# Kernel optimization log

Hardware: AMD Instinct MI355X
Metric: run time of the kernel (lower is better)

The kernel has to match this reference:

```python
import jax, jax.numpy as jnp
import numpy as np

N_FFT = 1024
HOP = 256
WIN = 1024
N_MELS = 80
SR = 22050
F_MIN = 0.0
CUTOFF = N_FFT // 2 + 1  # 513
PAD = (N_FFT - HOP) // 2  # 384
LOG_CLIP = 1e-5
B, T = 32, 262144


def _hann_periodic(n):
    return (0.5 - 0.5 * np.cos(2.0 * np.pi * np.arange(n) / n)).astype(np.float64)


def _hz_to_mel(f):
    f = np.atleast_1d(np.asarray(f, dtype=np.float64))
    f_sp = 200.0 / 3
    mels = f / f_sp
    min_log_hz = 1000.0
    min_log_mel = min_log_hz / f_sp
    logstep = np.log(6.4) / 27.0
    log_t = f >= min_log_hz
    mels[log_t] = min_log_mel + np.log(f[log_t] / min_log_hz) / logstep
    return mels


def _mel_to_hz(m):
    m = np.asarray(m, dtype=np.float64)
    f_sp = 200.0 / 3
    freqs = m * f_sp
    min_log_hz = 1000.0
    min_log_mel = min_log_hz / f_sp
    logstep = np.log(6.4) / 27.0
    log_t = m >= min_log_mel
    freqs = np.where(log_t, min_log_hz * np.exp(logstep * (m - min_log_mel)), freqs)
    return freqs


def _mel_filterbank(sr, n_fft, n_mels, fmin, fmax):
    # librosa.filters.mel with htk=False, norm='slaney'
    if fmax is None:
        fmax = sr / 2.0
    mel_f = _mel_to_hz(np.linspace(_hz_to_mel(fmin)[0], _hz_to_mel(fmax)[0], n_mels + 2))
    fftfreqs = np.linspace(0.0, sr / 2.0, 1 + n_fft // 2)
    fdiff = np.diff(mel_f)
    ramps = mel_f[:, None] - fftfreqs[None, :]
    lower = -ramps[:-2] / fdiff[:-1, None]
    upper = ramps[2:] / fdiff[1:, None]
    weights = np.maximum(0.0, np.minimum(lower, upper))
    enorm = 2.0 / (mel_f[2:n_mels + 2] - mel_f[:n_mels])
    weights *= enorm[:, None]
    return weights.astype(np.float32)  # [n_mels, cutoff]


def _forward_basis():
    # Windowed real/imag DFT basis, as in the torch module.
    fourier = np.fft.fft(np.eye(N_FFT))
    basis = np.vstack([np.real(fourier[:CUTOFF, :]), np.imag(fourier[:CUTOFF, :])])
    basis = basis * _hann_periodic(WIN)[None, :]
    return basis.astype(np.float32)  # [2*cutoff, n_fft]


def setup_inputs() -> dict:
    key = jax.random.key(0)
    audio = jax.random.uniform(key, (B, T), dtype=jnp.float32, minval=-1.0, maxval=1.0)
    return {
        "audio": audio,
        "forward_basis": jnp.asarray(_forward_basis()),
        "mel_basis": jnp.asarray(_mel_filterbank(SR, N_FFT, N_MELS, F_MIN, None)),
        "jitter_steps": 0,
    }


def reference(audio, forward_basis, mel_basis, jitter_steps):
    # jitter_steps == 0 at eval: no random shift applied.
    padded = jnp.pad(audio, ((0, 0), (PAD, PAD)), mode="reflect")  # [B, T+2*PAD]
    n_frames = (padded.shape[-1] - N_FFT) // HOP + 1
    idx = jnp.arange(n_frames)[:, None] * HOP + jnp.arange(N_FFT)[None, :]
    frames = padded[:, idx]  # [B, n_frames, n_fft]
    ft = jnp.einsum("btn,cn->bct", frames, forward_basis)  # [B, 2*cutoff, n_frames]
    real, imag = ft[:, :CUTOFF, :], ft[:, CUTOFF:, :]
    mag = jnp.sqrt(real * real + imag * imag)  # [B, cutoff, n_frames]
    mel = jnp.einsum("mc,bct->bmt", mel_basis, mag)  # [B, n_mels, n_frames]
    return jnp.log(jnp.clip(mel, LOG_CLIP, None))
```

## Files before the change

kernel.cpp:

```cpp
#include <hip/hip_runtime.h>
#include <hip/hip_bf16.h>

typedef short bf16x8 __attribute__((ext_vector_type(8)));
typedef float f32x4  __attribute__((ext_vector_type(4)));
typedef int   i32x4  __attribute__((ext_vector_type(4)));

#define T_AUDIO 262144
#define PADL 384
#define CUTOFF 513
#define CPAD 576
#define NMELS 80
#define SEGLEN 33536
#define EBYTES 33536

__device__ __forceinline__ unsigned short f2bf(float f){
  union { float f; unsigned u; } v; v.f = f;
  return (unsigned short)((v.u + 0x7FFFu + ((v.u >> 16) & 1u)) >> 16);
}

__device__ __forceinline__ void gload_lds16(const void* g, void* l){
  __builtin_amdgcn_global_load_lds(
      (const __attribute__((address_space(1))) unsigned int*)g,
      (__attribute__((address_space(3))) unsigned int*)l, 16, 0, 0);
}

__global__ void k_extra(const float* __restrict__ audio,
                        const float* __restrict__ basis,
                        unsigned short* __restrict__ magT){
  __shared__ float swr[4], swi[4];
  int tid = threadIdx.x;
  int gid = blockIdx.x * 256 + tid;
  int b   = gid >> 17;
  int rem = gid & 131071;
  int t   = rem >> 7;
  int k0  = (rem & 127) << 3;
  int s0  = t * 256 + k0 - PADL;
  const float* ap = audio + (long)b * T_AUDIO;
  float v[8];
  if (s0 >= 0 && s0 + 7 < T_AUDIO){
    f32x4 a0 = *(const f32x4*)(ap + s0);
    f32x4 a1 = *(const f32x4*)(ap + s0 + 4);
    v[0]=a0[0]; v[1]=a0[1]; v[2]=a0[2]; v[3]=a0[3];
    v[4]=a1[0]; v[5]=a1[1]; v[6]=a1[2]; v[7]=a1[3];
  } else {
    #pragma unroll
    for (int e = 0; e < 8; ++e){
      int s = s0 + e;
      if (s < 0) s = -s;
      if (s >= T_AUDIO) s = 2*(T_AUDIO-1) - s;
      v[e] = ap[s];
    }
  }
  const float* r256 = basis + 256 * 1024 + k0;
  const float* i256 = basis + 769 * 1024 + k0;
  float dr = 0.f, di = 0.f;
  #pragma unroll
  for (int e = 0; e < 8; ++e){ dr += v[e]*r256[e]; di += v[e]*i256[e]; }
  #pragma unroll
  for (int off = 32; off; off >>= 1){
    dr += __shfl_down(dr, off, 64);
    di += __shfl_down(di, off, 64);
  }
  int lane = tid & 63, wid = tid >> 6;
  if (lane == 0){ swr[wid] = dr; swi[wid] = di; }
  __syncthreads();
  long tg = (long)b * 1024 + t;
  if (tid == 0 || tid == 128){
    float R = (tid == 0) ? (swr[0] + swr[1]) : (swr[2] + swr[3]);
    float I = (tid == 0) ? (swi[0] + swi[1]) : (swi[2] + swi[3]);
    magT[tg * CPAD + 256] = f2bf(sqrtf(R*R + I*I));
  }
  int c = tid & 127;
  if (c < 63){
    int p = (c < 7) ? (257 + c) : (513 + c);
    magT[tg * CPAD + p] = 0;
  }
}

__global__ void k_basis4(const float* __restrict__ basis, unsigned short* __restrict__ bi2f){
  int CI = blockIdx.x * 256 + threadIdx.x;
  int l  = CI & 63;
  int f  = (CI >> 6) & 7;
  int s  = (CI >> 9) & 15;
  int p  = (CI >> 13) & 1;
  int g  = CI >> 14;
  int R  = g * 128 + (f >> 2) * 64 + (f & 3) * 16 + (l & 15);
  int srcr = (R >> 1) + 513 * (R & 1);
  const float* sp = basis + srcr * 1024 + 2 * (s * 32 + (l >> 4) * 8) + p;
  bf16x8 o;
  #pragma unroll
  for (int e = 0; e < 8; ++e) o[e] = (short)f2bf(sp[2*e]);
  *(bf16x8*)(bi2f + (long)CI * 8) = o;
}

__global__ void k_w(const float* __restrict__ w, unsigned short* __restrict__ wb){
  int gid = blockIdx.x * 256 + threadIdx.x;
  if (gid >= NMELS * CPAD) return;
  int m = gid / CPAD, p = gid % CPAD;
  float v = 0.f;
  if (p <= 256) v = w[m * CUTOFF + p];
  else if (p >= 264 && p <= 519) v = w[m * CUTOFF + (p - 7)];
  wb[gid] = f2bf(v);
}

__launch_bounds__(256, 2)
__global__ void k_stft(const unsigned short* __restrict__ bi2f,
                       const float* __restrict__ audio,
                       unsigned short* __restrict__ magT){
  __shared__ __align__(16) char LDS[2 * EBYTES];
  const int tid = threadIdx.x;
  const int l   = tid & 63, w = tid >> 6;
  const int wm  = w >> 1, wn = w & 1;
  const int x   = l & 15, h = l >> 4;

  int bx = blockIdx.x;
  int sw = ((bx & 7) << 7) | (bx >> 3);
  const int g  = sw & 3;
  const int nt = sw >> 2;

  {
    const long segbase = (long)(nt >> 3) * T_AUDIO;
    const int  f0 = (nt & 7) << 7;
    const int  sstart = f0 * 256 - PADL;
    const float* ap = audio + segbase;
    #pragma unroll
    for (int it = 0; it < 17; ++it){
      int p0 = (it * 256 + tid) * 8;
      if (p0 < SEGLEN){
        int sg = sstart + p0;
        float v[8];
        if (sg >= 0 && sg + 7 < T_AUDIO){
          f32x4 a0 = *(const f32x4*)(ap + sg);
          f32x4 a1 = *(const f32x4*)(ap + sg + 4);
          v[0]=a0[0]; v[1]=a0[1]; v[2]=a0[2]; v[3]=a0[3];
          v[4]=a1[0]; v[5]=a1[1]; v[6]=a1[2]; v[7]=a1[3];
        } else {
          #pragma unroll
          for (int e = 0; e < 8; ++e){
            int ss = sg + e;
            if (ss < 0) ss = -ss;
            if (ss >= T_AUDIO) ss = 2*(T_AUDIO-1) - ss;
            v[e] = ap[ss];
          }
        }
        unsigned long long pe = (unsigned long long)f2bf(v[0])
                              | ((unsigned long long)f2bf(v[2]) << 16)
                              | ((unsigned long long)f2bf(v[4]) << 32)
                              | ((unsigned long long)f2bf(v[6]) << 48);
        unsigned long long po = (unsigned long long)f2bf(v[1])
                              | ((unsigned long long)f2bf(v[3]) << 16)
                              | ((unsigned long long)f2bf(v[5]) << 32)
                              | ((unsigned long long)f2bf(v[7]) << 48);
        int ep = p0 >> 1;
        int C  = ep >> 3;
        int ad = ((C ^ ((C >> 4) & 15)) << 4) + ((ep & 4) << 1);
        *(unsigned long long*)(LDS + ad)          = pe;
        *(unsigned long long*)(LDS + EBYTES + ad) = po;
      }
    }
  }
  __syncthreads();

  const char* AgE = (const char*)bi2f + (long)(g * 256 + wm * 4) * 1024 + l * 16;
  const char* AgO = AgE + 131072;

  int C0[4];
  #pragma unroll
  for (int j = 0; j < 4; ++j) C0[j] = (wn * 64 + j * 16 + x) * 16 + h;

  f32x4 accE[4][4] = {}, accO[4][4] = {};
  bf16x8 aE[2][4], aO[2][4];
  #pragma unroll
  for (int i = 0; i < 4; ++i){
    aE[0][i] = *(const bf16x8*)(AgE + i * 1024);
    aO[0][i] = *(const bf16x8*)(AgO + i * 1024);
  }

  #pragma unroll
  for (int s = 0; s < 16; ++s){
    const int cur = s & 1, nxt = cur ^ 1;
    if (s < 15){
      #pragma unroll
      for (int i = 0; i < 4; ++i){
        aE[nxt][i] = *(const bf16x8*)(AgE + (s + 1) * 8192 + i * 1024);
        aO[nxt][i] = *(const bf16x8*)(AgO + (s + 1) * 8192 + i * 1024);
      }
    }
    bf16x8 bqE[4], bqO[4];
    #pragma unroll
    for (int j = 0; j < 4; ++j){
      int C  = C0[j] + s * 4;
      int ad = (C ^ ((C >> 4) & 15)) << 4;
      bqE[j] = *(const bf16x8*)(LDS + ad);
      bqO[j] = *(const bf16x8*)(LDS + EBYTES + ad);
    }
    __builtin_amdgcn_s_setprio(1);
    #pragma unroll
    for (int i = 0; i < 4; ++i)
      #pragma unroll
      for (int j = 0; j < 4; ++j)
        accE[i][j] = __builtin_amdgcn_mfma_f32_16x16x32_bf16(aE[cur][i], bqE[j], accE[i][j], 0, 0, 0);
    #pragma unroll
    for (int i = 0; i < 4; ++i)
      #pragma unroll
      for (int j = 0; j < 4; ++j)
        accO[i][j] = __builtin_amdgcn_mfma_f32_16x16x32_bf16(aO[cur][i], bqO[j], accO[i][j], 0, 0, 0);
    __builtin_amdgcn_s_setprio(0);
  }

  __syncthreads();
  #pragma unroll
  for (int i = 0; i < 4; ++i){
    int cp1 = wm * 16 + i * 4 + h;
    int mp  = 63 - cp1;
    #pragma unroll
    for (int j = 0; j < 4; ++j){
      int tl = wn * 64 + j * 16 + x;
      f32x4 E = accE[i][j], O = accO[i][j];
      float m1 = sqrtf((E[0]+O[0])*(E[0]+O[0]) + (E[1]+O[1])*(E[1]+O[1]));
      float m2 = sqrtf((E[2]+O[2])*(E[2]+O[2]) + (E[3]+O[3])*(E[3]+O[3]));
      float m3 = sqrtf((E[0]-O[0])*(E[0]-O[0]) + (E[1]-O[1])*(E[1]-O[1]));
      float m4 = sqrtf((E[2]-O[2])*(E[2]-O[2]) + (E[3]-O[3])*(E[3]-O[3]));
      unsigned p1 = (unsigned)f2bf(m1) | ((unsigned)f2bf(m2) << 16);
      unsigned p2 = (unsigned)f2bf(m4) | ((unsigned)f2bf(m3) << 16);
      int xs = (tl & 7) << 2;
      *(unsigned*)(LDS + tl * 256 + ((cp1 ^ xs) << 2)) = p1;
      *(unsigned*)(LDS + tl * 256 + ((mp  ^ xs) << 2)) = p2;
    }
  }
  __syncthreads();

  {
    const long rowbase = (long)(nt * 128) * CPAD;
    int slot8 = tid & 15, rr = tid >> 4;
    int cb0 = (slot8 < 8) ? (64 * g + slot8 * 8) : (392 - 64 * g + slot8 * 8);
    #pragma unroll
    for (int pass = 0; pass < 8; ++pass){
      int tl = pass * 16 + rr;
      int f4 = (slot8 * 4) ^ ((tl & 7) << 2);
      i32x4 vv = *(const i32x4*)(LDS + tl * 256 + f4 * 4);
      *(i32x4*)((char*)magT + (rowbase + (long)tl * CPAD + cb0) * 2) = vv;
    }
  }
}

__launch_bounds__(256)
__global__ void k_mel(const unsigned short* __restrict__ wb,
                      const unsigned short* __restrict__ magT,
                      float* __restrict__ out){
  __shared__ unsigned short Ws[80 * 32];
  __shared__ unsigned short Ms[128 * 32];
  int tid  = threadIdx.x, lane = tid & 63, wid = tid >> 6;
  int bx   = blockIdx.x;
  int bt   = bx & 7, b = bx >> 3;
  int t0   = bt * 128;
  f32x4 acc[5][2] = {};
  const char* Mb = (const char*)(magT + ((long)b * 1024 + t0) * CPAD);
  const char* Wb = (const char*)wb;

  for (int kt = 0; kt < 18; ++kt){
    int k0b = kt * 64;
    {
      int o = tid * 16;
      gload_lds16(Wb + (o >> 6) * 1152 + k0b + (o & 63), (char*)Ws + wid * 1024);
      if (wid == 0){
        int o2 = 4096 + lane * 16;
        gload_lds16(Wb + (o2 >> 6) * 1152 + k0b + (o2 & 63), (char*)Ws + 4096);
      }
    }
    #pragma unroll
    for (int q = 0; q < 2; ++q){
      int o = (q * 256 + tid) * 16;
      gload_lds16(Mb + (long)(o >> 6) * 1152 + k0b + (o & 63), (char*)Ms + q * 4096 + wid * 1024);
    }
    __syncthreads();
    bf16x8 af[5], bfr[2];
    int kb = (lane >> 4) << 4;
    #pragma unroll
    for (int i = 0; i < 5; ++i)
      af[i] = *(const bf16x8*)((const char*)Ws + (i*16 + (lane & 15)) * 64 + kb);
    #pragma unroll
    for (int j = 0; j < 2; ++j)
      bfr[j] = *(const bf16x8*)((const char*)Ms + (wid*32 + j*16 + (lane & 15)) * 64 + kb);
    #pragma unroll
    for (int i = 0; i < 5; ++i)
      #pragma unroll
      for (int j = 0; j < 2; ++j)
        acc[i][j] = __builtin_amdgcn_mfma_f32_16x16x32_bf16(af[i], bfr[j], acc[i][j], 0, 0, 0);
    __syncthreads();
  }
  #pragma unroll
  for (int i = 0; i < 5; ++i)
    #pragma unroll
    for (int j = 0; j < 2; ++j){
      int m = i*16 + ((lane >> 4) << 2);
      int t = t0 + wid*32 + j*16 + (lane & 15);
      #pragma unroll
      for (int r = 0; r < 4; ++r){
        float v = acc[i][j][r];
        out[((long)b * NMELS + (m + r)) * 1024 + t] = logf(fmaxf(v, 1e-5f));
      }
    }
}

__global__ void k_sentinel(float* out, int n){
  int i = blockIdx.x * 256 + threadIdx.x;
  if (i < n) out[i] = 12345.0f;
}

extern "C" void kernel_launch(void* const* d_in, const int* in_sizes, int n_in,
                              void* d_out, int out_size, void* d_ws, size_t ws_size,
                              hipStream_t stream){
  const float* audio = (const float*)d_in[0];
  const float* basis = (const float*)d_in[1];
  const float* melw  = (const float*)d_in[2];
  float* out = (float*)d_out;

  size_t off_bi  = 0;
  size_t off_wb  = (size_t)1024 * 1024;
  size_t off_mag = off_wb + (size_t)NMELS * CPAD * 2;
  size_t total   = off_mag + (size_t)32 * 1024 * CPAD * 2;

  if (ws_size < total){
    k_sentinel<<<(out_size + 255) / 256, 256, 0, stream>>>(out, out_size);
    return;
  }
  char* ws = (char*)d_ws;
  unsigned short* bi2f = (unsigned short*)(ws + off_bi);
  unsigned short* wb   = (unsigned short*)(ws + off_wb);
  unsigned short* magT = (unsigned short*)(ws + off_mag);

  k_extra <<<16384, 256, 0, stream>>>(audio, basis, magT);
  k_basis4<<<  256, 256, 0, stream>>>(basis, bi2f);
  k_w     <<<  180, 256, 0, stream>>>(melw, wb);
  k_stft  <<< 1024, 256, 0, stream>>>(bi2f, audio, magT);
  k_mel   <<<  256, 256, 0, stream>>>(wb, magT, out);
}
```

Before: 81.13 us.

## Double STFT frame tile per block to 256 frames, halving block count

```diff
diff --git a/kernel.cpp b/kernel.cpp
--- a/kernel.cpp
+++ b/kernel.cpp
@@ -10,8 +10,8 @@
 #define CUTOFF 513
 #define CPAD 576
 #define NMELS 80
-#define SEGLEN 33536
-#define EBYTES 33536
+#define SEGLEN2 66304
+#define EB2 66304
 
 __device__ __forceinline__ unsigned short f2bf(float f){
   union { float f; unsigned u; } v; v.f = f;
@@ -103,30 +103,29 @@
   wb[gid] = f2bf(v);
 }
 
-__launch_bounds__(256, 2)
+__launch_bounds__(256, 1)
 __global__ void k_stft(const unsigned short* __restrict__ bi2f,
                        const float* __restrict__ audio,
                        unsigned short* __restrict__ magT){
-  __shared__ __align__(16) char LDS[2 * EBYTES];
+  __shared__ __align__(16) char LDS[2 * EB2];
   const int tid = threadIdx.x;
   const int l   = tid & 63, w = tid >> 6;
   const int wm  = w >> 1, wn = w & 1;
   const int x   = l & 15, h = l >> 4;
 
   int bx = blockIdx.x;
-  int sw = ((bx & 7) << 7) | (bx >> 3);
-  const int g  = sw & 3;
-  const int nt = sw >> 2;
+  int sw = ((bx & 7) << 6) | (bx >> 3);
+  const int g   = sw & 3;
+  const int nt2 = sw >> 2;
 
   {
-    const long segbase = (long)(nt >> 3) * T_AUDIO;
-    const int  f0 = (nt & 7) << 7;
-    const int  sstart = f0 * 256 - PADL;
+    const long segbase = (long)(nt2 >> 2) * T_AUDIO;
+    const int  sstart  = ((nt2 & 3) << 16) - PADL;
     const float* ap = audio + segbase;
-    #pragma unroll
-    for (int it = 0; it < 17; ++it){
+    #pragma unroll 4
+    for (int it = 0; it < 33; ++it){
       int p0 = (it * 256 + tid) * 8;
-      if (p0 < SEGLEN){
+      if (p0 < SEGLEN2){
         int sg = sstart + p0;
         float v[8];
         if (sg >= 0 && sg + 7 < T_AUDIO){
@@ -154,8 +153,8 @@
         int ep = p0 >> 1;
         int C  = ep >> 3;
         int ad = ((C ^ ((C >> 4) & 15)) << 4) + ((ep & 4) << 1);
-        *(unsigned long long*)(LDS + ad)          = pe;
-        *(unsigned long long*)(LDS + EBYTES + ad) = po;
+        *(unsigned long long*)(LDS + ad)       = pe;
+        *(unsigned long long*)(LDS + EB2 + ad) = po;
       }
     }
   }
@@ -164,11 +163,11 @@
   const char* AgE = (const char*)bi2f + (long)(g * 256 + wm * 4) * 1024 + l * 16;
   const char* AgO = AgE + 131072;
 
-  int C0[4];
-  #pragma unroll
-  for (int j = 0; j < 4; ++j) C0[j] = (wn * 64 + j * 16 + x) * 16 + h;
-
-  f32x4 accE[4][4] = {}, accO[4][4] = {};
+  int C0[8];
+  #pragma unroll
+  for (int j = 0; j < 8; ++j) C0[j] = (wn * 128 + j * 16 + x) * 16 + h;
+
+  f32x4 accE[4][8] = {}, accO[4][8] = {};
   bf16x8 aE[2][4], aO[2][4];
   #pragma unroll
   for (int i = 0; i < 4; ++i){
@@ -186,24 +185,32 @@
         aO[nxt][i] = *(const bf16x8*)(AgO + (s + 1) * 8192 + i * 1024);
       }
     }
-    bf16x8 bqE[4], bqO[4];
-    #pragma unroll
-    for (int j = 0; j < 4; ++j){
+    bf16x8 bqE[8];
+    #pragma unroll
+    for (int j = 0; j < 8; ++j){
       int C  = C0[j] + s * 4;
       int ad = (C ^ ((C >> 4) & 15)) << 4;
       bqE[j] = *(const bf16x8*)(LDS + ad);
-      bqO[j] = *(const bf16x8*)(LDS + EBYTES + ad);
     }
     __builtin_amdgcn_s_setprio(1);
     #pragma unroll
     for (int i = 0; i < 4; ++i)
       #pragma unroll
-      for (int j = 0; j < 4; ++j)
+      for (int j = 0; j < 8; ++j)
         accE[i][j] = __builtin_amdgcn_mfma_f32_16x16x32_bf16(aE[cur][i], bqE[j], accE[i][j], 0, 0, 0);
+    __builtin_amdgcn_s_setprio(0);
+    bf16x8 bqO[8];
+    #pragma unroll
+    for (int j = 0; j < 8; ++j){
+      int C  = C0[j] + s * 4;
+      int ad = (C ^ ((C >> 4) & 15)) << 4;
+      bqO[j] = *(const bf16x8*)(LDS + EB2 + ad);
+    }
+    __builtin_amdgcn_s_setprio(1);
     #pragma unroll
     for (int i = 0; i < 4; ++i)
       #pragma unroll
-      for (int j = 0; j < 4; ++j)
+      for (int j = 0; j < 8; ++j)
         accO[i][j] = __builtin_amdgcn_mfma_f32_16x16x32_bf16(aO[cur][i], bqO[j], accO[i][j], 0, 0, 0);
     __builtin_amdgcn_s_setprio(0);
   }
@@ -214,8 +221,8 @@
     int cp1 = wm * 16 + i * 4 + h;
     int mp  = 63 - cp1;
     #pragma unroll
-    for (int j = 0; j < 4; ++j){
-      int tl = wn * 64 + j * 16 + x;
+    for (int j = 0; j < 8; ++j){
+      int tl = wn * 128 + j * 16 + x;
       f32x4 E = accE[i][j], O = accO[i][j];
       float m1 = sqrtf((E[0]+O[0])*(E[0]+O[0]) + (E[1]+O[1])*(E[1]+O[1]));
       float m2 = sqrtf((E[2]+O[2])*(E[2]+O[2]) + (E[3]+O[3])*(E[3]+O[3]));
@@ -231,11 +238,11 @@
   __syncthreads();
 
   {
-    const long rowbase = (long)(nt * 128) * CPAD;
+    const long rowbase = (long)(nt2 * 256) * CPAD;
     int slot8 = tid & 15, rr = tid >> 4;
     int cb0 = (slot8 < 8) ? (64 * g + slot8 * 8) : (392 - 64 * g + slot8 * 8);
     #pragma unroll
-    for (int pass = 0; pass < 8; ++pass){
+    for (int pass = 0; pass < 16; ++pass){
       int tl = pass * 16 + rr;
       int f4 = (slot8 * 4) ^ ((tl & 7) << 2);
       i32x4 vv = *(const i32x4*)(LDS + tl * 256 + f4 * 4);
@@ -333,6 +340,6 @@
   k_extra <<<16384, 256, 0, stream>>>(audio, basis, magT);
   k_basis4<<<  256, 256, 0, stream>>>(basis, bi2f);
   k_w     <<<  180, 256, 0, stream>>>(melw, wb);
-  k_stft  <<< 1024, 256, 0, stream>>>(bi2f, audio, magT);
+  k_stft  <<<  512, 256, 0, stream>>>(bi2f, audio, magT);
   k_mel   <<<  256, 256, 0, stream>>>(wb, magT, out);
 }
```

After: 107.6 us. 1.33x slower.

## Pre-convert audio to bf16 even/odd planes and async-load them into LDS

Applied to the files above, without the earlier changes.

```diff
diff --git a/kernel.cpp b/kernel.cpp
--- a/kernel.cpp
+++ b/kernel.cpp
@@ -12,10 +12,15 @@
 #define NMELS 80
 #define SEGLEN 33536
 #define EBYTES 33536
+#define PCH 16448
+#define PBYTES (PCH*16)
 
 __device__ __forceinline__ unsigned short f2bf(float f){
   union { float f; unsigned u; } v; v.f = f;
   return (unsigned short)((v.u + 0x7FFFu + ((v.u >> 16) & 1u)) >> 16);
+}
+__device__ __forceinline__ float bf2f(unsigned short u){
+  union { unsigned u; float f; } v; v.u = (unsigned)u << 16; return v.f;
 }
 
 __device__ __forceinline__ void gload_lds16(const void* g, void* l){
@@ -24,57 +29,38 @@
       (__attribute__((address_space(3))) unsigned int*)l, 16, 0, 0);
 }
 
-__global__ void k_extra(const float* __restrict__ audio,
-                        const float* __restrict__ basis,
-                        unsigned short* __restrict__ magT){
-  __shared__ float swr[4], swi[4];
-  int tid = threadIdx.x;
-  int gid = blockIdx.x * 256 + tid;
-  int b   = gid >> 17;
-  int rem = gid & 131071;
-  int t   = rem >> 7;
-  int k0  = (rem & 127) << 3;
-  int s0  = t * 256 + k0 - PADL;
+__global__ void k_audio(const float* __restrict__ audio, unsigned short* __restrict__ planes){
+  int bx = blockIdx.x;
+  int b  = bx / 65;
+  int ci = (bx % 65) * 256 + threadIdx.x;
+  if (ci >= PCH) return;
   const float* ap = audio + (long)b * T_AUDIO;
-  float v[8];
-  if (s0 >= 0 && s0 + 7 < T_AUDIO){
-    f32x4 a0 = *(const f32x4*)(ap + s0);
-    f32x4 a1 = *(const f32x4*)(ap + s0 + 4);
-    v[0]=a0[0]; v[1]=a0[1]; v[2]=a0[2]; v[3]=a0[3];
-    v[4]=a1[0]; v[5]=a1[1]; v[6]=a1[2]; v[7]=a1[3];
+  int s0 = 16 * ci - 384;
+  float v[16];
+  if (s0 >= 0 && s0 + 15 < T_AUDIO){
+    #pragma unroll
+    for (int q = 0; q < 4; ++q){
+      f32x4 a = *(const f32x4*)(ap + s0 + q * 4);
+      v[q*4]=a[0]; v[q*4+1]=a[1]; v[q*4+2]=a[2]; v[q*4+3]=a[3];
+    }
   } else {
     #pragma unroll
-    for (int e = 0; e < 8; ++e){
+    for (int e = 0; e < 16; ++e){
       int s = s0 + e;
       if (s < 0) s = -s;
       if (s >= T_AUDIO) s = 2*(T_AUDIO-1) - s;
       v[e] = ap[s];
     }
   }
-  const float* r256 = basis + 256 * 1024 + k0;
-  const float* i256 = basis + 769 * 1024 + k0;
-  float dr = 0.f, di = 0.f;
-  #pragma unroll
-  for (int e = 0; e < 8; ++e){ dr += v[e]*r256[e]; di += v[e]*i256[e]; }
-  #pragma unroll
-  for (int off = 32; off; off >>= 1){
-    dr += __shfl_down(dr, off, 64);
-    di += __shfl_down(di, off, 64);
-  }
-  int lane = tid & 63, wid = tid >> 6;
-  if (lane == 0){ swr[wid] = dr; swi[wid] = di; }
-  __syncthreads();
-  long tg = (long)b * 1024 + t;
-  if (tid == 0 || tid == 128){
-    float R = (tid == 0) ? (swr[0] + swr[1]) : (swr[2] + swr[3]);
-    float I = (tid == 0) ? (swi[0] + swi[1]) : (swi[2] + swi[3]);
-    magT[tg * CPAD + 256] = f2bf(sqrtf(R*R + I*I));
-  }
-  int c = tid & 127;
-  if (c < 63){
-    int p = (c < 7) ? (257 + c) : (513 + c);
-    magT[tg * CPAD + p] = 0;
-  }
+  bf16x8 ev, ov;
+  #pragma unroll
+  for (int e = 0; e < 8; ++e){
+    ev[e] = (short)f2bf(v[2*e]);
+    ov[e] = (short)f2bf(v[2*e+1]);
+  }
+  unsigned short* pE = planes + (long)b * 2 * (PCH * 8);
+  *(bf16x8*)(pE + (long)ci * 8)            = ev;
+  *(bf16x8*)(pE + PCH * 8 + (long)ci * 8)  = ov;
 }
 
 __global__ void k_basis4(const float* __restrict__ basis, unsigned short* __restrict__ bi2f){
@@ -93,19 +79,57 @@
   *(bf16x8*)(bi2f + (long)CI * 8) = o;
 }
 
-__global__ void k_w(const float* __restrict__ w, unsigned short* __restrict__ wb){
+__global__ void k_w(const float* __restrict__ w, const float* __restrict__ basis,
+                    unsigned short* __restrict__ wb, float* __restrict__ beo){
   int gid = blockIdx.x * 256 + threadIdx.x;
-  if (gid >= NMELS * CPAD) return;
-  int m = gid / CPAD, p = gid % CPAD;
-  float v = 0.f;
-  if (p <= 256) v = w[m * CUTOFF + p];
-  else if (p >= 264 && p <= 519) v = w[m * CUTOFF + (p - 7)];
-  wb[gid] = f2bf(v);
+  if (gid < NMELS * CPAD){
+    int m = gid / CPAD, p = gid % CPAD;
+    float v = 0.f;
+    if (p <= 256) v = w[m * CUTOFF + p];
+    else if (p >= 264 && p <= 519) v = w[m * CUTOFF + (p - 7)];
+    wb[gid] = f2bf(v);
+  } else {
+    int g2 = gid - NMELS * CPAD;
+    int par = g2 >> 9, m = g2 & 511;
+    beo[g2] = par ? basis[769 * 1024 + 2*m + 1] : basis[256 * 1024 + 2*m];
+  }
+}
+
+__global__ void k_extra(const unsigned short* __restrict__ planes,
+                        const float* __restrict__ beo,
+                        unsigned short* __restrict__ magT){
+  int tid = threadIdx.x, l = tid & 63, w = tid >> 6;
+  long fr = (long)blockIdx.x * 4 + w;
+  int b = (int)(fr >> 10), t = (int)(fr & 1023);
+  const unsigned short* pE = planes + (long)b * 2 * (PCH * 8);
+  const unsigned short* pO = pE + PCH * 8;
+  int idx = t * 128 + l * 8;
+  bf16x8 ev = *(const bf16x8*)(pE + idx);
+  bf16x8 ov = *(const bf16x8*)(pO + idx);
+  f32x4 be0 = *(const f32x4*)(beo + l*8);
+  f32x4 be1 = *(const f32x4*)(beo + l*8 + 4);
+  f32x4 bo0 = *(const f32x4*)(beo + 512 + l*8);
+  f32x4 bo1 = *(const f32x4*)(beo + 512 + l*8 + 4);
+  float re = bf2f(ev[0])*be0[0] + bf2f(ev[1])*be0[1] + bf2f(ev[2])*be0[2] + bf2f(ev[3])*be0[3]
+           + bf2f(ev[4])*be1[0] + bf2f(ev[5])*be1[1] + bf2f(ev[6])*be1[2] + bf2f(ev[7])*be1[3];
+  float im = bf2f(ov[0])*bo0[0] + bf2f(ov[1])*bo0[1] + bf2f(ov[2])*bo0[2] + bf2f(ov[3])*bo0[3]
+           + bf2f(ov[4])*bo1[0] + bf2f(ov[5])*bo1[1] + bf2f(ov[6])*bo1[2] + bf2f(ov[7])*bo1[3];
+  #pragma unroll
+  for (int m = 1; m < 64; m <<= 1){
+    re += __shfl_xor(re, m, 64);
+    im += __shfl_xor(im, m, 64);
+  }
+  long tg = fr * CPAD;
+  if (l == 0) magT[tg + 256] = f2bf(sqrtf(re*re + im*im));
+  if (l < 63){
+    int p = (l < 7) ? (257 + l) : (513 + l);
+    magT[tg + p] = 0;
+  }
 }
 
 __launch_bounds__(256, 2)
 __global__ void k_stft(const unsigned short* __restrict__ bi2f,
-                       const float* __restrict__ audio,
+                       const unsigned short* __restrict__ planes,
                        unsigned short* __restrict__ magT){
   __shared__ __align__(16) char LDS[2 * EBYTES];
   const int tid = threadIdx.x;
@@ -119,46 +143,19 @@
   const int nt = sw >> 2;
 
   {
-    const long segbase = (long)(nt >> 3) * T_AUDIO;
-    const int  f0 = (nt & 7) << 7;
-    const int  sstart = f0 * 256 - PADL;
-    const float* ap = audio + segbase;
-    #pragma unroll
-    for (int it = 0; it < 17; ++it){
-      int p0 = (it * 256 + tid) * 8;
-      if (p0 < SEGLEN){
-        int sg = sstart + p0;
-        float v[8];
-        if (sg >= 0 && sg + 7 < T_AUDIO){
-          f32x4 a0 = *(const f32x4*)(ap + sg);
-          f32x4 a1 = *(const f32x4*)(ap + sg + 4);
-          v[0]=a0[0]; v[1]=a0[1]; v[2]=a0[2]; v[3]=a0[3];
-          v[4]=a1[0]; v[5]=a1[1]; v[6]=a1[2]; v[7]=a1[3];
-        } else {
-          #pragma unroll
-          for (int e = 0; e < 8; ++e){
-            int ss = sg + e;
-            if (ss < 0) ss = -ss;
-            if (ss >= T_AUDIO) ss = 2*(T_AUDIO-1) - ss;
-            v[e] = ap[ss];
-          }
-        }
-        unsigned long long pe = (unsigned long long)f2bf(v[0])
-                              | ((unsigned long long)f2bf(v[2]) << 16)
-                              | ((unsigned long long)f2bf(v[4]) << 32)
-                              | ((unsigned long long)f2bf(v[6]) << 48);
-        unsigned long long po = (unsigned long long)f2bf(v[1])
-                              | ((unsigned long long)f2bf(v[3]) << 16)
-                              | ((unsigned long long)f2bf(v[5]) << 32)
-                              | ((unsigned long long)f2bf(v[7]) << 48);
-        int ep = p0 >> 1;
-        int C  = ep >> 3;
-        int ad = ((C ^ ((C >> 4) & 15)) << 4) + ((ep & 4) << 1);
-        *(unsigned long long*)(LDS + ad)          = pe;
-        *(unsigned long long*)(LDS + EBYTES + ad) = po;
-      }
-    }
-  }
+    const char* pb = (const char*)planes + (long)(nt >> 3) * 2 * PBYTES;
+    const int k7o = (nt & 7) * 2048;
+    #pragma unroll
+    for (int it = 0; it < 9; ++it){
+      int o = it * 256 + tid;
+      if (o < 2096){
+        long so = (long)((o ^ ((o >> 4) & 15)) + k7o) * 16;
+        gload_lds16(pb + so,          LDS + o * 16);
+        gload_lds16(pb + PBYTES + so, LDS + EBYTES + o * 16);
+      }
+    }
+  }
+  asm volatile("s_waitcnt vmcnt(0)" ::: "memory");
   __syncthreads();
 
   const char* AgE = (const char*)bi2f + (long)(g * 256 + wm * 4) * 1024 + l * 16;
@@ -169,12 +166,18 @@
   for (int j = 0; j < 4; ++j) C0[j] = (wn * 64 + j * 16 + x) * 16 + h;
 
   f32x4 accE[4][4] = {}, accO[4][4] = {};
-  bf16x8 aE[2][4], aO[2][4];
+  bf16x8 aE[2][4], aO[2][4], bqE[4], bqO[4];
   #pragma unroll
   for (int i = 0; i < 4; ++i){
     aE[0][i] = *(const bf16x8*)(AgE + i * 1024);
     aO[0][i] = *(const bf16x8*)(AgO + i * 1024);
   }
+  #pragma unroll
+  for (int j = 0; j < 4; ++j){
+    int C = C0[j]; int ad = (C ^ ((C >> 4) & 15)) << 4;
+    bqE[j] = *(const bf16x8*)(LDS + ad);
+    bqO[j] = *(const bf16x8*)(LDS + EBYTES + ad);
+  }
 
   #pragma unroll
   for (int s = 0; s < 16; ++s){
@@ -186,26 +189,34 @@
         aO[nxt][i] = *(const bf16x8*)(AgO + (s + 1) * 8192 + i * 1024);
       }
     }
-    bf16x8 bqE[4], bqO[4];
-    #pragma unroll
-    for (int j = 0; j < 4; ++j){
-      int C  = C0[j] + s * 4;
-      int ad = (C ^ ((C >> 4) & 15)) << 4;
-      bqE[j] = *(const bf16x8*)(LDS + ad);
-      bqO[j] = *(const bf16x8*)(LDS + EBYTES + ad);
-    }
     __builtin_amdgcn_s_setprio(1);
     #pragma unroll
     for (int i = 0; i < 4; ++i)
       #pragma unroll
       for (int j = 0; j < 4; ++j)
         accE[i][j] = __builtin_amdgcn_mfma_f32_16x16x32_bf16(aE[cur][i], bqE[j], accE[i][j], 0, 0, 0);
+    __builtin_amdgcn_s_setprio(0);
+    if (s < 15){
+      #pragma unroll
+      for (int j = 0; j < 4; ++j){
+        int C = C0[j] + (s + 1) * 4; int ad = (C ^ ((C >> 4) & 15)) << 4;
+        bqE[j] = *(const bf16x8*)(LDS + ad);
+      }
+    }
+    __builtin_amdgcn_s_setprio(1);
     #pragma unroll
     for (int i = 0; i < 4; ++i)
       #pragma unroll
       for (int j = 0; j < 4; ++j)
         accO[i][j] = __builtin_amdgcn_mfma_f32_16x16x32_bf16(aO[cur][i], bqO[j], accO[i][j], 0, 0, 0);
     __builtin_amdgcn_s_setprio(0);
+    if (s < 15){
+      #pragma unroll
+      for (int j = 0; j < 4; ++j){
+        int C = C0[j] + (s + 1) * 4; int ad = (C ^ ((C >> 4) & 15)) << 4;
+        bqO[j] = *(const bf16x8*)(LDS + EBYTES + ad);
+      }
+    }
   }
 
   __syncthreads();
@@ -318,21 +329,26 @@
 
   size_t off_bi  = 0;
   size_t off_wb  = (size_t)1024 * 1024;
-  size_t off_mag = off_wb + (size_t)NMELS * CPAD * 2;
-  size_t total   = off_mag + (size_t)32 * 1024 * CPAD * 2;
+  size_t off_beo = off_wb + (size_t)NMELS * CPAD * 2;
+  size_t off_mag = off_beo + 1024 * 4;
+  size_t off_pl  = off_mag + (size_t)32 * 1024 * CPAD * 2;
+  size_t total   = off_pl + (size_t)32 * 2 * PBYTES;
 
   if (ws_size < total){
     k_sentinel<<<(out_size + 255) / 256, 256, 0, stream>>>(out, out_size);
     return;
   }
   char* ws = (char*)d_ws;
-  unsigned short* bi2f = (unsigned short*)(ws + off_bi);
-  unsigned short* wb   = (unsigned short*)(ws + off_wb);
-  unsigned short* magT = (unsigned short*)(ws + off_mag);
-
-  k_extra <<<16384, 256, 0, stream>>>(audio, basis, magT);
+  unsigned short* bi2f   = (unsigned short*)(ws + off_bi);
+  unsigned short* wb     = (unsigned short*)(ws + off_wb);
+  float*          beo    = (float*)(ws + off_beo);
+  unsigned short* magT   = (unsigned short*)(ws + off_mag);
+  unsigned short* planes = (unsigned short*)(ws + off_pl);
+
+  k_audio <<< 2080, 256, 0, stream>>>(audio, planes);
   k_basis4<<<  256, 256, 0, stream>>>(basis, bi2f);
-  k_w     <<<  180, 256, 0, stream>>>(melw, wb);
-  k_stft  <<< 1024, 256, 0, stream>>>(bi2f, audio, magT);
+  k_w     <<<  184, 256, 0, stream>>>(melw, basis, wb, beo);
+  k_extra <<< 8192, 256, 0, stream>>>(planes, beo, magT);
+  k_stft  <<< 1024, 256, 0, stream>>>(bi2f, planes, magT);
   k_mel   <<<  256, 256, 0, stream>>>(wb, magT, out);
 }
```

After: 77.56 us. 4.4% less time.
